# Performance work log

Measured on AMD Instinct MI355X. Metric: run time of the kernel, lower is better.

## Reference

```python
import jax, jax.numpy as jnp
import numpy as np

B, D, H, L = 131072, 64, 256, 8  # batch, input_dim, hidden_dim, n_coupling_layers


def _alternating_masks():
    m = np.zeros((L, D), np.float32)
    m[:, ::2] = 1.0            # even layers: mask = 1,0,1,0,...
    m[1::2] = 1.0 - m[1::2]    # odd layers:  mask = 0,1,0,1,...
    return jnp.asarray(m)


def setup_inputs() -> dict:
    key = jax.random.key(0)
    ks = jax.random.split(key, 14)

    def lin_w(k, o, i):
        return (jax.random.normal(k, (L, o, i), jnp.float32) / np.sqrt(i))

    return {
        "x": jax.random.normal(ks[0], (B, D), jnp.float32),
        "masks": _alternating_masks(),                      # [L, D]
        # scale network params (stacked over layers)
        "sW1": lin_w(ks[1], H, D), "sb1": jnp.zeros((L, H), jnp.float32),
        "sW2": lin_w(ks[2], H, H), "sb2": jnp.zeros((L, H), jnp.float32),
        "sW3": lin_w(ks[3], D, H), "sb3": jnp.zeros((L, D), jnp.float32),
        "scale": 0.1 * jax.random.normal(ks[4], (L, D), jnp.float32),
        # translation network params
        "tW1": lin_w(ks[5], H, D), "tb1": jnp.zeros((L, H), jnp.float32),
        "tW2": lin_w(ks[6], H, H), "tb2": jnp.zeros((L, H), jnp.float32),
        "tW3": lin_w(ks[7], D, H), "tb3": jnp.zeros((L, D), jnp.float32),
    }


def _flow(x, masks, sW1, sb1, sW2, sb2, sW3, sb3, scale,
          tW1, tb1, tW2, tb2, tW3, tb3):
    def layer(carry, p):
        y, ld = carry
        m, W1, b1, W2, b2, W3, b3, sc, V1, c1, V2, c2, V3, c3 = p
        xm = y * m                                   # masked input [B, D]
        # scale net: residual tanh MLP, ends with +xm then elementwise *sc
        s = jnp.tanh(xm @ W1.T + b1)
        s = jnp.tanh(s @ W2.T + b2 + s)
        s = (jnp.tanh(s @ W3.T + b3) + xm) * sc
        # translation net
        t = jnp.tanh(xm @ V1.T + c1)
        t = jnp.tanh(t @ V2.T + c2 + t)
        t = (t @ V3.T + c3) + xm
        y2 = m * y + (1.0 - m) * (y * jnp.exp(s) + t)
        ld2 = ld + jnp.sum((1.0 - m) * s, -1)
        return (y2, ld2), None

    init = (x, jnp.zeros(x.shape[0], x.dtype))
    xs = (masks, sW1, sb1, sW2, sb2, sW3, sb3, scale,
          tW1, tb1, tW2, tb2, tW3, tb3)
    (y, logdet), _ = jax.lax.scan(layer, init, xs)
    return y, logdet


def reference(x, masks, sW1, sb1, sW2, sb2, sW3, sb3, scale,
              tW1, tb1, tW2, tb2, tW3, tb3):
    return _flow(x, masks, sW1, sb1, sW2, sb2, sW3, sb3, scale,
                 tW1, tb1, tW2, tb2, tW3, tb3)
```

## Files before the change

kernel.cpp:

```cpp
#include <hip/hip_runtime.h>


#define BATCH    131072
#define DIM      64
#define HID      256
#define NLAYER   8
#define BM       64
#define NTHREADS 256

#define ACT_S  264
#define XMP_S  40

typedef _Float16 f16;
typedef __attribute__((ext_vector_type(8))) _Float16 f16x8;
typedef __attribute__((ext_vector_type(4))) _Float16 f16x4;
typedef __attribute__((ext_vector_type(2))) _Float16 f16x2;
typedef __attribute__((ext_vector_type(4))) float    f32x4;

#define TWO_LOG2E 2.8853900817779268f
#define LOG2E     1.4426950408889634f

__device__ __forceinline__ float tanh_fast(float x) {
  float e = __builtin_amdgcn_exp2f(x * TWO_LOG2E);
  return 1.f - 2.f * __builtin_amdgcn_rcpf(e + 1.f);
}

__device__ __forceinline__ f16x2 pk2(float a, float b) {
  return __builtin_bit_cast(f16x2, __builtin_amdgcn_cvt_pkrtz(a, b));
}

__device__ __forceinline__ f16x4 pk4(float a, float b, float c, float d) {
  f16x2 lo = pk2(a, b);
  f16x2 hi = pk2(c, d);
  f16x4 o; o[0] = lo[0]; o[1] = lo[1]; o[2] = hi[0]; o[3] = hi[1];
  return o;
}

__global__ void cvt4_kernel(const float* s0, f16* d0, const float* s1, f16* d1,
                            const float* s2, f16* d2, const float* s3, f16* d3) {
  int i = blockIdx.x * blockDim.x + threadIdx.x;
  const float* s; f16* d; int base; bool isW2;
  if      (i < 131072) { s = s0; d = d0; base = 0;      isW2 = true;  }
  else if (i < 163840) { s = s1; d = d1; base = 131072; isW2 = false; }
  else if (i < 294912) { s = s2; d = d2; base = 163840; isW2 = true;  }
  else                 { s = s3; d = d3; base = 294912; isW2 = false; }
  int k = i - base;
  float4 v = ((const float4*)s)[k];
  if (isW2) {
    const int row = (k >> 6) & 255;
    const int j0  = (k & 63) * 4;
    const int dr  = row - j0;
    if (dr == 0) v.x += 1.f;
    else if (dr == 1) v.y += 1.f;
    else if (dr == 2) v.z += 1.f;
    else if (dr == 3) v.w += 1.f;
  }
  ((f16x4*)d)[k] = pk4(v.x, v.y, v.z, v.w);
}

__global__ void cvtW1p_kernel(const float* sW1f, f16* dS,
                              const float* tW1f, f16* dT) {
  int i = blockIdx.x * blockDim.x + threadIdx.x;
  const float* s = (i < 32768) ? sW1f : tW1f;
  f16*         d = (i < 32768) ? dS   : dT;
  int j   = i & 32767;
  int l   = j >> 12;
  int rem = j & 4095;
  int h   = rem >> 4;
  int kq  = rem & 15;
  int par = l & 1;
  const float a = s[l * 16384 + h * 64 + 4 * kq + par];
  const float b = s[l * 16384 + h * 64 + 4 * kq + 2 + par];
  ((f16x2*)d)[j] = pk2(a, b);
}

__global__ __launch_bounds__(NTHREADS, 3) void flow_kernel(
    const float* __restrict__ x, const float* __restrict__ masks,
    const f16* __restrict__ wS1p, const f16* __restrict__ wS2, const f16* __restrict__ wS3,
    const float* __restrict__ sb1, const float* __restrict__ sb2, const float* __restrict__ sb3,
    const float* __restrict__ scl,
    const f16* __restrict__ wT1p, const f16* __restrict__ wT2, const f16* __restrict__ wT3,
    const float* __restrict__ tb1, const float* __restrict__ tb2, const float* __restrict__ tb3,
    float* __restrict__ y_out, float* __restrict__ ld_out)
{
  __shared__ __attribute__((aligned(16))) f16 act [BM * ACT_S];
  __shared__ __attribute__((aligned(16))) f16 xm_p[BM * XMP_S];
  float* ld_red = (float*)xm_p;
  (void)masks;

  const int tid  = threadIdx.x;
  const int lane = tid & 63;
  const int wv   = tid >> 6;
  const int quad = lane >> 4;
  const int l16  = lane & 15;
  const int row0 = blockIdx.x * BM;
  const int d0   = wv * 16 + quad * 4;
  const int dp   = d0 >> 1;

  float yv [4][4];
  float s3r[4][2];
  float lda[4];
  #pragma unroll
  for (int n = 0; n < 4; ++n) {
    const float4 v = *(const float4*)&x[(size_t)(row0 + n * 16 + l16) * DIM + d0];
    yv[n][0] = v.x; yv[n][1] = v.y; yv[n][2] = v.z; yv[n][3] = v.w;
    lda[n] = 0.f;
  }

  #pragma unroll 1
  for (int l = 0; l < NLAYER; ++l) {
    const int par = l & 1;

    if (par == 0) {
      #pragma unroll
      for (int n = 0; n < 4; ++n)
        *(f16x2*)&xm_p[(n * 16 + l16) * XMP_S + dp] = pk2(yv[n][0], yv[n][2]);
    } else {
      #pragma unroll
      for (int n = 0; n < 4; ++n)
        *(f16x2*)&xm_p[(n * 16 + l16) * XMP_S + dp] = pk2(yv[n][1], yv[n][3]);
    }
    __syncthreads();

    #pragma unroll 1
    for (int net = 0; net < 2; ++net) {
      const f16*   W1 = (net ? wT1p : wS1p) + l * HID * 32;
      const f16*   W2 = (net ? wT2  : wS2)  + l * HID * HID;
      const f16*   W3 = (net ? wT3  : wS3)  + l * DIM * HID;
      const float* b1 = (net ? tb1 : sb1) + l * HID;
      const float* b2 = (net ? tb2 : sb2) + l * HID;
      const float* b3 = (net ? tb3 : sb3) + l * DIM;

      f32x4 acc[4][4];

      #pragma unroll
      for (int m = 0; m < 4; ++m) {
        const float4 bv = *(const float4*)&b1[wv * 64 + m * 16 + quad * 4];
        f32x4 bi; bi[0] = bv.x; bi[1] = bv.y; bi[2] = bv.z; bi[3] = bv.w;
        #pragma unroll
        for (int n = 0; n < 4; ++n) acc[m][n] = bi;
      }
      {
        f16x8 afr[4];
        #pragma unroll
        for (int m = 0; m < 4; ++m)
          afr[m] = *(const f16x8*)&W1[(wv * 64 + m * 16 + l16) * 32 + quad * 8];
        __builtin_amdgcn_s_setprio(1);
        #pragma unroll
        for (int n = 0; n < 4; ++n) {
          const f16x8 bfr = *(const f16x8*)&xm_p[(n * 16 + l16) * XMP_S + quad * 8];
          #pragma unroll
          for (int m = 0; m < 4; ++m)
            acc[m][n] = __builtin_amdgcn_mfma_f32_16x16x32_f16(afr[m], bfr, acc[m][n], 0, 0, 0);
        }
        __builtin_amdgcn_s_setprio(0);
      }
      #pragma unroll
      for (int m = 0; m < 4; ++m) {
        const int h0 = wv * 64 + m * 16 + quad * 4;
        #pragma unroll
        for (int n = 0; n < 4; ++n)
          *(f16x4*)&act[(n * 16 + l16) * ACT_S + h0] =
              pk4(tanh_fast(acc[m][n][0]), tanh_fast(acc[m][n][1]),
                  tanh_fast(acc[m][n][2]), tanh_fast(acc[m][n][3]));
      }
      __syncthreads();

      #pragma unroll
      for (int m = 0; m < 4; ++m) {
        const float4 bv = *(const float4*)&b2[wv * 64 + m * 16 + quad * 4];
        f32x4 bi; bi[0] = bv.x; bi[1] = bv.y; bi[2] = bv.z; bi[3] = bv.w;
        #pragma unroll
        for (int n = 0; n < 4; ++n) acc[m][n] = bi;
      }
      __builtin_amdgcn_s_setprio(1);
      #pragma unroll 2
      for (int kt = 0; kt < 8; ++kt) {
        const int k0 = kt * 32 + quad * 8;
        f16x8 afr[4];
        #pragma unroll
        for (int m = 0; m < 4; ++m)
          afr[m] = *(const f16x8*)&W2[(wv * 64 + m * 16 + l16) * HID + k0];
        #pragma unroll
        for (int n = 0; n < 4; ++n) {
          const f16x8 bfr = *(const f16x8*)&act[(n * 16 + l16) * ACT_S + k0];
          #pragma unroll
          for (int m = 0; m < 4; ++m)
            acc[m][n] = __builtin_amdgcn_mfma_f32_16x16x32_f16(afr[m], bfr, acc[m][n], 0, 0, 0);
        }
      }
      __builtin_amdgcn_s_setprio(0);
      __syncthreads();
      #pragma unroll
      for (int m = 0; m < 4; ++m) {
        const int h0 = wv * 64 + m * 16 + quad * 4;
        #pragma unroll
        for (int n = 0; n < 4; ++n)
          *(f16x4*)&act[(n * 16 + l16) * ACT_S + h0] =
              pk4(tanh_fast(acc[m][n][0]), tanh_fast(acc[m][n][1]),
                  tanh_fast(acc[m][n][2]), tanh_fast(acc[m][n][3]));
      }
      __syncthreads();

      f32x4 acc3[4];
      {
        const float4 bv = *(const float4*)&b3[d0];
        f32x4 bi; bi[0] = bv.x; bi[1] = bv.y; bi[2] = bv.z; bi[3] = bv.w;
        #pragma unroll
        for (int n = 0; n < 4; ++n) acc3[n] = bi;
      }
      __builtin_amdgcn_s_setprio(1);
      #pragma unroll 2
      for (int kt = 0; kt < 8; ++kt) {
        const int k0  = kt * 32 + quad * 8;
        const f16x8 a3 = *(const f16x8*)&W3[(wv * 16 + l16) * HID + k0];
        #pragma unroll
        for (int n = 0; n < 4; ++n) {
          const f16x8 bfr = *(const f16x8*)&act[(n * 16 + l16) * ACT_S + k0];
          acc3[n] = __builtin_amdgcn_mfma_f32_16x16x32_f16(a3, bfr, acc3[n], 0, 0, 0);
        }
      }
      __builtin_amdgcn_s_setprio(0);
      if (net == 0) __syncthreads();

      if (net == 0) {
        const float4 sv = *(const float4*)&scl[l * DIM + d0];
        if (par == 0) {
          #pragma unroll
          for (int n = 0; n < 4; ++n) {
            s3r[n][0] = tanh_fast(acc3[n][1]) * sv.y;
            s3r[n][1] = tanh_fast(acc3[n][3]) * sv.w;
          }
        } else {
          #pragma unroll
          for (int n = 0; n < 4; ++n) {
            s3r[n][0] = tanh_fast(acc3[n][0]) * sv.x;
            s3r[n][1] = tanh_fast(acc3[n][2]) * sv.z;
          }
        }
      } else {
        #define EP3I(n, r, SS) {                                         \
          const float s = (SS);                                          \
          const float e = __builtin_amdgcn_exp2f(s * LOG2E);             \
          yv[n][r] = yv[n][r] * e + acc3[n][r];                          \
          lda[n] += s; }
        if (par == 0) {
          #pragma unroll
          for (int n = 0; n < 4; ++n) {
            EP3I(n, 1, s3r[n][0])
            EP3I(n, 3, s3r[n][1])
          }
        } else {
          #pragma unroll
          for (int n = 0; n < 4; ++n) {
            EP3I(n, 0, s3r[n][0])
            EP3I(n, 2, s3r[n][1])
          }
        }
        #undef EP3I
      }
    }
  }

  #pragma unroll
  for (int n = 0; n < 4; ++n) {
    float4 v; v.x = yv[n][0]; v.y = yv[n][1]; v.z = yv[n][2]; v.w = yv[n][3];
    *(float4*)&y_out[(size_t)(row0 + n * 16 + l16) * DIM + d0] = v;
  }

  float v0 = lda[0], v1 = lda[1], v2 = lda[2], v3 = lda[3];
  v0 += __shfl_xor(v0, 16); v0 += __shfl_xor(v0, 32);
  v1 += __shfl_xor(v1, 16); v1 += __shfl_xor(v1, 32);
  v2 += __shfl_xor(v2, 16); v2 += __shfl_xor(v2, 32);
  v3 += __shfl_xor(v3, 16); v3 += __shfl_xor(v3, 32);
  __syncthreads();
  if (quad == 0) {
    ld_red[(0 * 16 + l16) * 4 + wv] = v0;
    ld_red[(1 * 16 + l16) * 4 + wv] = v1;
    ld_red[(2 * 16 + l16) * 4 + wv] = v2;
    ld_red[(3 * 16 + l16) * 4 + wv] = v3;
  }
  __syncthreads();
  if (tid < BM)
    ld_out[row0 + tid] = ld_red[tid * 4 + 0] + ld_red[tid * 4 + 1]
                       + ld_red[tid * 4 + 2] + ld_red[tid * 4 + 3];
}

extern "C" void kernel_launch(void* const* d_in, const int* in_sizes, int n_in,
                              void* d_out, int out_size, void* d_ws, size_t ws_size,
                              hipStream_t stream) {
  const float* x     = (const float*)d_in[0];
  const float* masks = (const float*)d_in[1];
  const float* sW1f  = (const float*)d_in[2];
  const float* sb1   = (const float*)d_in[3];
  const float* sW2f  = (const float*)d_in[4];
  const float* sb2   = (const float*)d_in[5];
  const float* sW3f  = (const float*)d_in[6];
  const float* sb3   = (const float*)d_in[7];
  const float* scl   = (const float*)d_in[8];
  const float* tW1f  = (const float*)d_in[9];
  const float* tb1   = (const float*)d_in[10];
  const float* tW2f  = (const float*)d_in[11];
  const float* tb2   = (const float*)d_in[12];
  const float* tW3f  = (const float*)d_in[13];
  const float* tb3   = (const float*)d_in[14];
  (void)in_sizes; (void)n_in; (void)out_size; (void)ws_size;

  const int W1PSZ = NLAYER * HID * 32;
  const int W2SZ  = NLAYER * HID * HID;
  const int W3SZ  = NLAYER * DIM * HID;
  f16* wS1p = (f16*)d_ws;
  f16* wS2  = wS1p + W1PSZ;
  f16* wS3  = wS2 + W2SZ;
  f16* wT1p = wS3 + W3SZ;
  f16* wT2  = wT1p + W1PSZ;
  f16* wT3  = wT2 + W2SZ;

  cvt4_kernel<<<1280, 256, 0, stream>>>(sW2f, wS2, sW3f, wS3, tW2f, wT2, tW3f, wT3);
  cvtW1p_kernel<<<256, 256, 0, stream>>>(sW1f, wS1p, tW1f, wT1p);

  float* y_out  = (float*)d_out;
  float* ld_out = y_out + (size_t)BATCH * DIM;
  flow_kernel<<<BATCH / BM, NTHREADS, 0, stream>>>(
      x, masks, wS1p, wS2, wS3, sb1, sb2, sb3, scl,
      wT1p, wT2, wT3, tb1, tb2, tb3, y_out, ld_out);
}
```

Before: 784.9 us.

## Compute only unmasked output columns in third GEMM via packed W3

W3 is pre-packed so that only the 32 output dimensions that get updated in each layer (the unmasked half) are kept. The third GEMM then issues half as many MFMAs, with waves split into 2 column tiles by 2 row halves. Register state is reorganised into even and odd column halves, and the masked-input staging moves to the end of each layer. The risk is extra index arithmetic and scalar bias and scale loads, and the third GEMM was already a small share of the total work.

```diff
diff --git a/kernel.cpp b/kernel.cpp
--- a/kernel.cpp
+++ b/kernel.cpp
@@ -36,50 +36,58 @@
   return o;
 }
 
-__global__ void cvt4_kernel(const float* s0, f16* d0, const float* s1, f16* d1,
-                            const float* s2, f16* d2, const float* s3, f16* d3) {
+__global__ void cvtW2_kernel(const float* s0, f16* d0, const float* s1, f16* d1) {
   int i = blockIdx.x * blockDim.x + threadIdx.x;
-  const float* s; f16* d; int base; bool isW2;
-  if      (i < 131072) { s = s0; d = d0; base = 0;      isW2 = true;  }
-  else if (i < 163840) { s = s1; d = d1; base = 131072; isW2 = false; }
-  else if (i < 294912) { s = s2; d = d2; base = 163840; isW2 = true;  }
-  else                 { s = s3; d = d3; base = 294912; isW2 = false; }
-  int k = i - base;
+  const float* s = (i < 131072) ? s0 : s1;
+  f16*         d = (i < 131072) ? d0 : d1;
+  int k = i & 131071;
   float4 v = ((const float4*)s)[k];
-  if (isW2) {
-    const int row = (k >> 6) & 255;
-    const int j0  = (k & 63) * 4;
-    const int dr  = row - j0;
-    if (dr == 0) v.x += 1.f;
-    else if (dr == 1) v.y += 1.f;
-    else if (dr == 2) v.z += 1.f;
-    else if (dr == 3) v.w += 1.f;
-  }
+  const int row = (k >> 6) & 255;
+  const int j0  = (k & 63) * 4;
+  const int dr  = row - j0;
+  if      (dr == 0) v.x += 1.f;
+  else if (dr == 1) v.y += 1.f;
+  else if (dr == 2) v.z += 1.f;
+  else if (dr == 3) v.w += 1.f;
   ((f16x4*)d)[k] = pk4(v.x, v.y, v.z, v.w);
 }
 
-__global__ void cvtW1p_kernel(const float* sW1f, f16* dS,
-                              const float* tW1f, f16* dT) {
+__global__ void cvtpack_kernel(const float* sW1f, f16* dS1, const float* tW1f, f16* dT1,
+                               const float* sW3f, f16* dS3, const float* tW3f, f16* dT3) {
   int i = blockIdx.x * blockDim.x + threadIdx.x;
-  const float* s = (i < 32768) ? sW1f : tW1f;
-  f16*         d = (i < 32768) ? dS   : dT;
-  int j   = i & 32767;
-  int l   = j >> 12;
-  int rem = j & 4095;
-  int h   = rem >> 4;
-  int kq  = rem & 15;
-  int par = l & 1;
-  const float a = s[l * 16384 + h * 64 + 4 * kq + par];
-  const float b = s[l * 16384 + h * 64 + 4 * kq + 2 + par];
-  ((f16x2*)d)[j] = pk2(a, b);
+  if (i < 65536) {
+    const float* s = (i < 32768) ? sW1f : tW1f;
+    f16*         d = (i < 32768) ? dS1  : dT1;
+    int j   = i & 32767;
+    int l   = j >> 12;
+    int rem = j & 4095;
+    int h   = rem >> 4;
+    int kq  = rem & 15;
+    int par = l & 1;
+    const float a = s[l * 16384 + h * 64 + 4 * kq + par];
+    const float b = s[l * 16384 + h * 64 + 4 * kq + 2 + par];
+    ((f16x2*)d)[j] = pk2(a, b);
+  } else {
+    int k = i - 65536;
+    const float* s = (k < 16384) ? sW3f : tW3f;
+    f16*         d = (k < 16384) ? dS3  : dT3;
+    int j2  = k & 16383;
+    int l   = j2 >> 11;
+    int rem = j2 & 2047;
+    int j   = rem >> 6;
+    int kq  = rem & 63;
+    int dd  = 2 * j + 1 - (l & 1);
+    float4 v = ((const float4*)s)[l * 4096 + dd * 64 + kq];
+    ((f16x4*)d)[j2] = pk4(v.x, v.y, v.z, v.w);
+  }
 }
 
 __global__ __launch_bounds__(NTHREADS, 3) void flow_kernel(
     const float* __restrict__ x, const float* __restrict__ masks,
-    const f16* __restrict__ wS1p, const f16* __restrict__ wS2, const f16* __restrict__ wS3,
+    const f16* __restrict__ wS1p, const f16* __restrict__ wS2, const f16* __restrict__ wS3p,
     const float* __restrict__ sb1, const float* __restrict__ sb2, const float* __restrict__ sb3,
     const float* __restrict__ scl,
-    const f16* __restrict__ wT1p, const f16* __restrict__ wT2, const f16* __restrict__ wT3,
+    const f16* __restrict__ wT1p, const f16* __restrict__ wT2, const f16* __restrict__ wT3p,
     const float* __restrict__ tb1, const float* __restrict__ tb2, const float* __restrict__ tb3,
     float* __restrict__ y_out, float* __restrict__ ld_out)
 {
@@ -94,39 +102,39 @@
   const int quad = lane >> 4;
   const int l16  = lane & 15;
   const int row0 = blockIdx.x * BM;
-  const int d0   = wv * 16 + quad * 4;
-  const int dp   = d0 >> 1;
-
-  float yv [4][4];
-  float s3r[4][2];
-  float lda[4];
+  const int jt   = wv & 1;
+  const int np   = wv >> 1;
+  const int j0   = jt * 16 + quad * 4;
+
+  float yE[2][4], yO[2][4];
+  float s3r[2][4];
+  float lda[2];
+  lda[0] = 0.f; lda[1] = 0.f;
+
   #pragma unroll
-  for (int n = 0; n < 4; ++n) {
-    const float4 v = *(const float4*)&x[(size_t)(row0 + n * 16 + l16) * DIM + d0];
-    yv[n][0] = v.x; yv[n][1] = v.y; yv[n][2] = v.z; yv[n][3] = v.w;
-    lda[n] = 0.f;
-  }
+  for (int n2 = 0; n2 < 2; ++n2) {
+    const size_t base = (size_t)(row0 + np * 32 + n2 * 16 + l16) * DIM + 2 * j0;
+    const float4 v0 = *(const float4*)&x[base];
+    const float4 v1 = *(const float4*)&x[base + 4];
+    yE[n2][0] = v0.x; yO[n2][0] = v0.y; yE[n2][1] = v0.z; yO[n2][1] = v0.w;
+    yE[n2][2] = v1.x; yO[n2][2] = v1.y; yE[n2][3] = v1.z; yO[n2][3] = v1.w;
+  }
+
+  #pragma unroll
+  for (int n2 = 0; n2 < 2; ++n2)
+    *(f16x4*)&xm_p[(np * 32 + n2 * 16 + l16) * XMP_S + j0] =
+        pk4(yE[n2][0], yE[n2][1], yE[n2][2], yE[n2][3]);
+  __syncthreads();
 
   #pragma unroll 1
   for (int l = 0; l < NLAYER; ++l) {
     const int par = l & 1;
-
-    if (par == 0) {
-      #pragma unroll
-      for (int n = 0; n < 4; ++n)
-        *(f16x2*)&xm_p[(n * 16 + l16) * XMP_S + dp] = pk2(yv[n][0], yv[n][2]);
-    } else {
-      #pragma unroll
-      for (int n = 0; n < 4; ++n)
-        *(f16x2*)&xm_p[(n * 16 + l16) * XMP_S + dp] = pk2(yv[n][1], yv[n][3]);
-    }
-    __syncthreads();
 
     #pragma unroll 1
     for (int net = 0; net < 2; ++net) {
       const f16*   W1 = (net ? wT1p : wS1p) + l * HID * 32;
       const f16*   W2 = (net ? wT2  : wS2)  + l * HID * HID;
-      const f16*   W3 = (net ? wT3  : wS3)  + l * DIM * HID;
+      const f16*   W3 = (net ? wT3p : wS3p) + l * 32 * HID;
       const float* b1 = (net ? tb1 : sb1) + l * HID;
       const float* b2 = (net ? tb2 : sb2) + l * HID;
       const float* b3 = (net ? tb3 : sb3) + l * DIM;
@@ -202,88 +210,93 @@
       }
       __syncthreads();
 
-      f32x4 acc3[4];
+      f32x4 acc3[2];
       {
-        const float4 bv = *(const float4*)&b3[d0];
-        f32x4 bi; bi[0] = bv.x; bi[1] = bv.y; bi[2] = bv.z; bi[3] = bv.w;
-        #pragma unroll
-        for (int n = 0; n < 4; ++n) acc3[n] = bi;
+        const int dj = 2 * j0 + 1 - par;
+        f32x4 bi;
+        bi[0] = b3[dj]; bi[1] = b3[dj + 2]; bi[2] = b3[dj + 4]; bi[3] = b3[dj + 6];
+        acc3[0] = bi; acc3[1] = bi;
       }
       __builtin_amdgcn_s_setprio(1);
       #pragma unroll 2
       for (int kt = 0; kt < 8; ++kt) {
         const int k0  = kt * 32 + quad * 8;
-        const f16x8 a3 = *(const f16x8*)&W3[(wv * 16 + l16) * HID + k0];
-        #pragma unroll
-        for (int n = 0; n < 4; ++n) {
-          const f16x8 bfr = *(const f16x8*)&act[(n * 16 + l16) * ACT_S + k0];
-          acc3[n] = __builtin_amdgcn_mfma_f32_16x16x32_f16(a3, bfr, acc3[n], 0, 0, 0);
+        const f16x8 a3 = *(const f16x8*)&W3[(jt * 16 + l16) * HID + k0];
+        #pragma unroll
+        for (int n2 = 0; n2 < 2; ++n2) {
+          const f16x8 bfr = *(const f16x8*)&act[(np * 32 + n2 * 16 + l16) * ACT_S + k0];
+          acc3[n2] = __builtin_amdgcn_mfma_f32_16x16x32_f16(a3, bfr, acc3[n2], 0, 0, 0);
         }
       }
       __builtin_amdgcn_s_setprio(0);
       if (net == 0) __syncthreads();
 
       if (net == 0) {
-        const float4 sv = *(const float4*)&scl[l * DIM + d0];
-        if (par == 0) {
-          #pragma unroll
-          for (int n = 0; n < 4; ++n) {
-            s3r[n][0] = tanh_fast(acc3[n][1]) * sv.y;
-            s3r[n][1] = tanh_fast(acc3[n][3]) * sv.w;
-          }
-        } else {
-          #pragma unroll
-          for (int n = 0; n < 4; ++n) {
-            s3r[n][0] = tanh_fast(acc3[n][0]) * sv.x;
-            s3r[n][1] = tanh_fast(acc3[n][2]) * sv.z;
-          }
+        const int dj = 2 * j0 + 1 - par;
+        const float sc0 = scl[l * DIM + dj];
+        const float sc1 = scl[l * DIM + dj + 2];
+        const float sc2 = scl[l * DIM + dj + 4];
+        const float sc3 = scl[l * DIM + dj + 6];
+        #pragma unroll
+        for (int n2 = 0; n2 < 2; ++n2) {
+          s3r[n2][0] = tanh_fast(acc3[n2][0]) * sc0;
+          s3r[n2][1] = tanh_fast(acc3[n2][1]) * sc1;
+          s3r[n2][2] = tanh_fast(acc3[n2][2]) * sc2;
+          s3r[n2][3] = tanh_fast(acc3[n2][3]) * sc3;
         }
       } else {
-        #define EP3I(n, r, SS) {                                         \
-          const float s = (SS);                                          \
-          const float e = __builtin_amdgcn_exp2f(s * LOG2E);             \
-          yv[n][r] = yv[n][r] * e + acc3[n][r];                          \
-          lda[n] += s; }
-        if (par == 0) {
-          #pragma unroll
-          for (int n = 0; n < 4; ++n) {
-            EP3I(n, 1, s3r[n][0])
-            EP3I(n, 3, s3r[n][1])
+        #define EP3U(Y)                                                  \
+          _Pragma("unroll")                                              \
+          for (int n2 = 0; n2 < 2; ++n2) {                               \
+            _Pragma("unroll")                                            \
+            for (int r = 0; r < 4; ++r) {                                \
+              const float s = s3r[n2][r];                                \
+              const float e = __builtin_amdgcn_exp2f(s * LOG2E);         \
+              Y[n2][r] = Y[n2][r] * e + acc3[n2][r];                     \
+              lda[n2] += s;                                              \
+            }                                                            \
           }
-        } else {
-          #pragma unroll
-          for (int n = 0; n < 4; ++n) {
-            EP3I(n, 0, s3r[n][0])
-            EP3I(n, 2, s3r[n][1])
-          }
-        }
-        #undef EP3I
+        if (par == 0) { EP3U(yO) } else { EP3U(yE) }
+        #undef EP3U
       }
     }
+
+    if (l + 1 < NLAYER) {
+      if (((l + 1) & 1) == 0) {
+        #pragma unroll
+        for (int n2 = 0; n2 < 2; ++n2)
+          *(f16x4*)&xm_p[(np * 32 + n2 * 16 + l16) * XMP_S + j0] =
+              pk4(yE[n2][0], yE[n2][1], yE[n2][2], yE[n2][3]);
+      } else {
+        #pragma unroll
+        for (int n2 = 0; n2 < 2; ++n2)
+          *(f16x4*)&xm_p[(np * 32 + n2 * 16 + l16) * XMP_S + j0] =
+              pk4(yO[n2][0], yO[n2][1], yO[n2][2], yO[n2][3]);
+      }
+    }
+    __syncthreads();
   }
 
   #pragma unroll
-  for (int n = 0; n < 4; ++n) {
-    float4 v; v.x = yv[n][0]; v.y = yv[n][1]; v.z = yv[n][2]; v.w = yv[n][3];
-    *(float4*)&y_out[(size_t)(row0 + n * 16 + l16) * DIM + d0] = v;
-  }
-
-  float v0 = lda[0], v1 = lda[1], v2 = lda[2], v3 = lda[3];
+  for (int n2 = 0; n2 < 2; ++n2) {
+    const size_t base = (size_t)(row0 + np * 32 + n2 * 16 + l16) * DIM + 2 * j0;
+    float4 v0, v1;
+    v0.x = yE[n2][0]; v0.y = yO[n2][0]; v0.z = yE[n2][1]; v0.w = yO[n2][1];
+    v1.x = yE[n2][2]; v1.y = yO[n2][2]; v1.z = yE[n2][3]; v1.w = yO[n2][3];
+    *(float4*)&y_out[base]     = v0;
+    *(float4*)&y_out[base + 4] = v1;
+  }
+
+  float v0 = lda[0], v1 = lda[1];
   v0 += __shfl_xor(v0, 16); v0 += __shfl_xor(v0, 32);
   v1 += __shfl_xor(v1, 16); v1 += __shfl_xor(v1, 32);
-  v2 += __shfl_xor(v2, 16); v2 += __shfl_xor(v2, 32);
-  v3 += __shfl_xor(v3, 16); v3 += __shfl_xor(v3, 32);
-  __syncthreads();
   if (quad == 0) {
-    ld_red[(0 * 16 + l16) * 4 + wv] = v0;
-    ld_red[(1 * 16 + l16) * 4 + wv] = v1;
-    ld_red[(2 * 16 + l16) * 4 + wv] = v2;
-    ld_red[(3 * 16 + l16) * 4 + wv] = v3;
+    ld_red[(np * 32 +      l16) * 2 + jt] = v0;
+    ld_red[(np * 32 + 16 + l16) * 2 + jt] = v1;
   }
   __syncthreads();
   if (tid < BM)
-    ld_out[row0 + tid] = ld_red[tid * 4 + 0] + ld_red[tid * 4 + 1]
-                       + ld_red[tid * 4 + 2] + ld_red[tid * 4 + 3];
+    ld_out[row0 + tid] = ld_red[tid * 2 + 0] + ld_red[tid * 2 + 1];
 }
 
 extern "C" void kernel_launch(void* const* d_in, const int* in_sizes, int n_in,
@@ -308,20 +321,21 @@
 
   const int W1PSZ = NLAYER * HID * 32;
   const int W2SZ  = NLAYER * HID * HID;
-  const int W3SZ  = NLAYER * DIM * HID;
+  const int W3PSZ = NLAYER * 32 * HID;
   f16* wS1p = (f16*)d_ws;
   f16* wS2  = wS1p + W1PSZ;
-  f16* wS3  = wS2 + W2SZ;
-  f16* wT1p = wS3 + W3SZ;
+  f16* wS3p = wS2 + W2SZ;
+  f16* wT1p = wS3p + W3PSZ;
   f16* wT2  = wT1p + W1PSZ;
-  f16* wT3  = wT2 + W2SZ;
-
-  cvt4_kernel<<<1280, 256, 0, stream>>>(sW2f, wS2, sW3f, wS3, tW2f, wT2, tW3f, wT3);
-  cvtW1p_kernel<<<256, 256, 0, stream>>>(sW1f, wS1p, tW1f, wT1p);
+  f16* wT3p = wT2 + W2SZ;
+
+  cvtW2_kernel<<<1024, 256, 0, stream>>>(sW2f, wS2, tW2f, wT2);
+  cvtpack_kernel<<<384, 256, 0, stream>>>(sW1f, wS1p, tW1f, wT1p,
+                                          sW3f, wS3p, tW3f, wT3p);
 
   float* y_out  = (float*)d_out;
   float* ld_out = y_out + (size_t)BATCH * DIM;
   flow_kernel<<<BATCH / BM, NTHREADS, 0, stream>>>(
-      x, masks, wS1p, wS2, wS3, sb1, sb2, sb3, scl,
-      wT1p, wT2, wT3, tb1, tb2, tb3, y_out, ld_out);
-}
+      x, masks, wS1p, wS2, wS3p, sb1, sb2, sb3, scl,
+      wT1p, wT2, wT3p, tb1, tb2, tb3, y_out, ld_out);
+}
```

Measured after the change: 775.1 us. About the same (-1.3%).
